# Kernel optimization log

Hardware: AMD Instinct MI355X
Metric: run time of the kernel (lower is better)

The kernel has to match this reference:

```python
import jax, jax.numpy as jnp
import numpy as np

ALPHA = 0.5
REG_RATIO = 0.5


def _xavier(key, shape):
    fan_in, fan_out = shape
    lim = np.sqrt(6.0 / (fan_in + fan_out))
    return jax.random.uniform(key, shape, minval=-lim, maxval=lim, dtype=jnp.float32)


def setup_inputs() -> dict:
    key = jax.random.key(0)
    ks = jax.random.split(key, 5)
    B, T, I, H, O = 128, 512, 4, 512, 3
    return {
        "x": jax.random.normal(ks[0], (B, T, I), dtype=jnp.float32),
        "h": jax.random.normal(ks[1], (B, H), dtype=jnp.float32),
        "W_rec": _xavier(ks[2], (H, H)),
        "W_in": _xavier(ks[3], (I, H)),
        "W_out": _xavier(ks[4], (H, O)),
        "bias_rec": jnp.zeros((H,), dtype=jnp.float32),
        "bias_in": jnp.zeros((H,), dtype=jnp.float32),
    }


def reference(x, h, W_rec, W_in, W_out, bias_rec, bias_in):
    # x: (B, T, I), h: (B, H)
    B, T, _ = x.shape
    H = h.shape[1]
    n_reg = round(H * REG_RATIO)
    alpha = jnp.asarray(ALPHA, x.dtype)
    # add_noise=False -> noise term is zero
    xt = jnp.swapaxes(x, 0, 1)                     # (T, B, I)
    flags = (jnp.arange(T) > 0).astype(x.dtype)    # z_old reg term skipped at t=0

    def step(carry, inp):
        h_prev, z_prev, reg = carry
        x_t, flag = inp
        # z = W_rec-recurrence + input drive (h_rec + h_in in the torch code)
        z_new = jnp.tanh(h_prev) @ W_rec + bias_rec + x_t @ W_in + bias_in  # (B, H)
        h_new = (1.0 - alpha) * h_prev + alpha * z_new
        # note: h_from_prev / (1 - alpha) == h_prev
        reg = (reg
               + jnp.sum((h_new[:, :n_reg] - h_prev[:, :n_reg]) ** 2)
               + flag * jnp.sum((z_new[:, :n_reg] - z_prev[:, :n_reg]) ** 2))
        out = h_new @ W_out                        # (B, O)
        return (h_new, z_new, reg), (h_new, out)

    init = (h, jnp.zeros_like(h), jnp.asarray(0.0, x.dtype))
    (_, _, reg), (hs, outs) = jax.lax.scan(step, init, (xt, flags))

    hidden_states = jnp.concatenate([h[None], hs], axis=0)  # (T+1, B, H)
    outputs = jnp.swapaxes(outs, 0, 1)                      # (B, T, O)
    tcr_reg = reg / T / B / n_reg
    return outputs, hidden_states, tcr_reg
```

## Files before the change

### kernel.cpp

```cpp
#include <hip/hip_runtime.h>
#include <math.h>


#define BB 128
#define TT 512
#define II 4
#define HH 512
#define OO 3
#define NREG_ 256

#define NTHREADS 512
#define MEMBERS 4
#define ROWS 2
#define NGROUPS 64
#define NBLOCKS (NGROUPS * MEMBERS)

typedef unsigned long long u64;
typedef unsigned int u32;

__device__ __forceinline__ u64 aload(const u64* p) {
    return __hip_atomic_load(p, __ATOMIC_RELAXED, __HIP_MEMORY_SCOPE_AGENT);
}
__device__ __forceinline__ void astore(u64* p, u64 v) {
    __hip_atomic_store(p, v, __ATOMIC_RELAXED, __HIP_MEMORY_SCOPE_AGENT);
}
__device__ __forceinline__ float rlane(float v, int l) {
    return __uint_as_float(__builtin_amdgcn_readlane(__float_as_uint(v), l));
}

#define R16(M) M(0) M(1) M(2) M(3) M(4) M(5) M(6) M(7) \
               M(8) M(9) M(10) M(11) M(12) M(13) M(14) M(15)

#define WLD(Q) \
    float4 wa##Q, wb##Q; \
    wa##Q.x = Wp[(size_t)(4*Q+0)*HH];      wa##Q.y = Wp[(size_t)(4*Q+1)*HH]; \
    wa##Q.z = Wp[(size_t)(4*Q+2)*HH];      wa##Q.w = Wp[(size_t)(4*Q+3)*HH]; \
    wb##Q.x = Wp[(size_t)(4*Q+0)*HH + 64]; wb##Q.y = Wp[(size_t)(4*Q+1)*HH + 64]; \
    wb##Q.z = Wp[(size_t)(4*Q+2)*HH + 64]; wb##Q.w = Wp[(size_t)(4*Q+3)*HH + 64];

#define MV(Q) \
    { float s0 = rlane(ar0, 4*Q+0), s1 = rlane(ar1, 4*Q+0); \
      acc00 = fmaf(s0, wa##Q.x, acc00); acc01 = fmaf(s0, wb##Q.x, acc01); \
      acc10 = fmaf(s1, wa##Q.x, acc10); acc11 = fmaf(s1, wb##Q.x, acc11); } \
    { float s0 = rlane(ar0, 4*Q+1), s1 = rlane(ar1, 4*Q+1); \
      acc00 = fmaf(s0, wa##Q.y, acc00); acc01 = fmaf(s0, wb##Q.y, acc01); \
      acc10 = fmaf(s1, wa##Q.y, acc10); acc11 = fmaf(s1, wb##Q.y, acc11); } \
    { float s0 = rlane(ar0, 4*Q+2), s1 = rlane(ar1, 4*Q+2); \
      acc00 = fmaf(s0, wa##Q.z, acc00); acc01 = fmaf(s0, wb##Q.z, acc01); \
      acc10 = fmaf(s1, wa##Q.z, acc10); acc11 = fmaf(s1, wb##Q.z, acc11); } \
    { float s0 = rlane(ar0, 4*Q+3), s1 = rlane(ar1, 4*Q+3); \
      acc00 = fmaf(s0, wa##Q.w, acc00); acc01 = fmaf(s0, wb##Q.w, acc01); \
      acc10 = fmaf(s1, wa##Q.w, acc10); acc11 = fmaf(s1, wb##Q.w, acc11); }

__global__ __launch_bounds__(NTHREADS, 2)
void rnn_main(const float* __restrict__ x,
              const float* __restrict__ h0,
              const float* __restrict__ W_rec,
              const float* __restrict__ W_in,
              const float* __restrict__ bias_rec,
              const float* __restrict__ bias_in,
              float* __restrict__ hidden,
              u64* __restrict__ abuf,
              float* __restrict__ partials)
{
    const int tid  = threadIdx.x;
    const int bid  = blockIdx.x;
    const int xcd  = bid & 7;
    const int onx  = bid >> 3;
    const int memb = onx & (MEMBERS - 1);
    const int group = xcd * 8 + (onx >> 2);
    const int r0   = group * ROWS;
    const int wid  = tid >> 6;
    const int lane = tid & 63;

    __shared__ float sc_s[ROWS][128][9];
    __shared__ float xbuf[ROWS * TT * II];
    __shared__ float win_s[II][128];
    __shared__ float ub_s[128];
    __shared__ float red_s[NTHREADS / 64];

    for (int idx = tid; idx < ROWS * TT * II; idx += NTHREADS) {
        int r = idx >> 11, rem = idx & (TT * II - 1);
        xbuf[idx] = x[(size_t)(r0 + r) * (TT * II) + rem];
    }
    if (tid < II * 128) {
        int i = tid >> 7, jj = tid & 127;
        win_s[i][jj] = W_in[i * HH + memb * 128 + jj];
    }
    if (tid < 128) {
        ub_s[tid] = bias_rec[memb * 128 + tid] + bias_in[memb * 128 + tid];
    }

    const float* Wp = W_rec + (size_t)(wid * 64) * HH + memb * 128 + lane;
    R16(WLD)

    const int fr  = tid >> 7;
    const int fj  = tid & 127;
    const int fjg = memb * 128 + fj;
    float hprev = 0.0f, zprev = 0.0f, racc = 0.0f;
    if (tid < ROWS * 128) {
        hprev = h0[(size_t)(r0 + fr) * HH + fjg];
        float a0v = tanhf(hprev);
        u64 pv = (u64)__float_as_uint(a0v) | ((u64)1u << 32);
        astore(&abuf[((size_t)(0 * BB + r0 + fr)) * HH + fjg], pv);
        hidden[(size_t)(r0 + fr) * HH + fjg] = hprev;
    }

#pragma unroll 1
    for (int t = 0; t < TT; ++t) {
        const int  slot = t & 1;
        const u32  tagc = (u32)(t + 1);
        const u32  tagp = (u32)(t + 2);

        const u64* p0 = abuf + ((size_t)(slot * BB + r0)) * HH + wid * 64 + lane;
        const u64* p1 = p0 + HH;
        u64 u0, u1;
        for (;;) {
            u0 = aload(p0);
            u1 = aload(p1);
            bool ok = ((u32)(u0 >> 32) == tagc) & ((u32)(u1 >> 32) == tagc);
            if (__all(ok)) break;
        }
        float ar0 = __uint_as_float((u32)u0);
        float ar1 = __uint_as_float((u32)u1);

        float acc00 = 0.0f, acc01 = 0.0f, acc10 = 0.0f, acc11 = 0.0f;
        R16(MV)

        sc_s[0][lane][wid]      = acc00;
        sc_s[0][lane + 64][wid] = acc01;
        sc_s[1][lane][wid]      = acc10;
        sc_s[1][lane + 64][wid] = acc11;
        __syncthreads();

        if (tid < ROWS * 128) {
            float q0 = sc_s[fr][fj][0], q1 = sc_s[fr][fj][1];
            float q2 = sc_s[fr][fj][2], q3 = sc_s[fr][fj][3];
            float q4 = sc_s[fr][fj][4], q5 = sc_s[fr][fj][5];
            float q6 = sc_s[fr][fj][6], q7 = sc_s[fr][fj][7];
            float z = ((q0 + q1) + (q2 + q3)) + ((q4 + q5) + (q6 + q7));
            z += ub_s[fj];
            const float* xr = &xbuf[fr * (TT * II) + t * II];
            z = fmaf(xr[0], win_s[0][fj], z);
            z = fmaf(xr[1], win_s[1][fj], z);
            z = fmaf(xr[2], win_s[2][fj], z);
            z = fmaf(xr[3], win_s[3][fj], z);
            float hn = 0.5f * hprev + 0.5f * z;
            float av = tanhf(hn);
            u64 pv = (u64)__float_as_uint(av) | ((u64)tagp << 32);
            astore(&abuf[((size_t)(((t + 1) & 1) * BB + r0 + fr)) * HH + fjg], pv);
            hidden[(size_t)(t + 1) * BB * HH + (size_t)(r0 + fr) * HH + fjg] = hn;
            if (fjg < NREG_) {
                float d1 = hn - hprev;
                racc = fmaf(d1, d1, racc);
                if (t > 0) { float d2 = z - zprev; racc = fmaf(d2, d2, racc); }
                zprev = z;
            }
            hprev = hn;
        }
        __syncthreads();
    }

    for (int off = 32; off; off >>= 1) racc += __shfl_down(racc, off);
    if ((tid & 63) == 0) red_s[tid >> 6] = racc;
    __syncthreads();
    if (tid == 0) {
        float s = 0.0f;
        for (int i = 0; i < NTHREADS / 64; ++i) s += red_s[i];
        partials[bid] = s;
    }
}

__global__ __launch_bounds__(256)
void rnn_out(const float* __restrict__ hidden,
             const float* __restrict__ W_out,
             float* __restrict__ outputs)
{
    __shared__ float wout_s[HH * OO];
    const int tid = threadIdx.x;
    for (int i = tid; i < HH * OO; i += 256) wout_s[i] = W_out[i];
    __syncthreads();

    const int gid  = blockIdx.x * 4 + (tid >> 6);
    const int lane = tid & 63;
    const int b = gid >> 9;
    const int t = gid & (TT - 1);
    const float* hp = hidden + (size_t)(t + 1) * BB * HH + (size_t)b * HH;

    float o0 = 0.0f, o1 = 0.0f, o2 = 0.0f;
#pragma unroll
    for (int q = 0; q < 8; ++q) {
        int k = lane + 64 * q;
        float hv = hp[k];
        o0 = fmaf(hv, wout_s[k * 3 + 0], o0);
        o1 = fmaf(hv, wout_s[k * 3 + 1], o1);
        o2 = fmaf(hv, wout_s[k * 3 + 2], o2);
    }
    for (int off = 32; off; off >>= 1) {
        o0 += __shfl_down(o0, off);
        o1 += __shfl_down(o1, off);
        o2 += __shfl_down(o2, off);
    }
    if (lane == 0) {
        float* op = outputs + (size_t)(b * TT + t) * OO;
        op[0] = o0; op[1] = o1; op[2] = o2;
    }
}

__global__ __launch_bounds__(256)
void rnn_tcr(const float* __restrict__ partials, float* __restrict__ tcr)
{
    __shared__ float red[4];
    const int tid = threadIdx.x;
    float v = partials[tid];
    for (int off = 32; off; off >>= 1) v += __shfl_down(v, off);
    if ((tid & 63) == 0) red[tid >> 6] = v;
    __syncthreads();
    if (tid == 0) {
        float s = red[0] + red[1] + red[2] + red[3];
        *tcr = s * (1.0f / ((float)TT * (float)BB * (float)NREG_));
    }
}

extern "C" void kernel_launch(void* const* d_in, const int* in_sizes, int n_in,
                              void* d_out, int out_size, void* d_ws, size_t ws_size,
                              hipStream_t stream)
{
    (void)in_sizes; (void)n_in; (void)out_size; (void)ws_size;

    const float* x     = (const float*)d_in[0];
    const float* h0    = (const float*)d_in[1];
    const float* W_rec = (const float*)d_in[2];
    const float* W_in  = (const float*)d_in[3];
    const float* W_out = (const float*)d_in[4];
    const float* brec  = (const float*)d_in[5];
    const float* bin   = (const float*)d_in[6];

    float* out     = (float*)d_out;
    float* outputs = out;
    float* hidden  = out + (size_t)BB * TT * OO;
    float* tcr     = out + (size_t)BB * TT * OO + (size_t)(TT + 1) * BB * HH;

    u64* abuf = (u64*)d_ws;
    const size_t abuf_bytes = (size_t)2 * BB * HH * sizeof(u64);
    float* partials = (float*)((char*)d_ws + abuf_bytes);

    (void)hipMemsetAsync(d_ws, 0, abuf_bytes, stream);

    void* args[] = { (void*)&x, (void*)&h0, (void*)&W_rec, (void*)&W_in,
                     (void*)&brec, (void*)&bin, (void*)&hidden,
                     (void*)&abuf, (void*)&partials };
    (void)hipLaunchCooperativeKernel((const void*)rnn_main,
                                     dim3(NBLOCKS), dim3(NTHREADS),
                                     args, 0, stream);

    rnn_out<<<dim3((BB * TT) / 4), dim3(256), 0, stream>>>(hidden, W_out, outputs);
    rnn_tcr<<<dim3(1), dim3(256), 0, stream>>>(partials, tcr);
}
```

Baseline: 1.212 ms.

## Use packed FMA for matvec, fast tanh, and double-buffer partials to drop a barrier

The inner mat-vec now uses inline v_pk_fma_f32 with a scalar pair of broadcast activations, halving the number of FMA instructions. tanhf is replaced by an exp/rcp approximation, which cuts latency on the serial critical path at some cost in accuracy. The shared-memory partial-sum buffer is double-buffered by timestep parity, so the second __syncthreads per step can be removed. The removal relies on the cross-block spin wait to keep warps from running more than one step ahead.

```diff
diff --git a/kernel.cpp b/kernel.cpp
--- a/kernel.cpp
+++ b/kernel.cpp
@@ -17,6 +17,7 @@
 
 typedef unsigned long long u64;
 typedef unsigned int u32;
+typedef __attribute__((ext_vector_type(2))) float f32x2;
 
 __device__ __forceinline__ u64 aload(const u64* p) {
     return __hip_atomic_load(p, __ATOMIC_RELAXED, __HIP_MEMORY_SCOPE_AGENT);
@@ -24,35 +25,35 @@
 __device__ __forceinline__ void astore(u64* p, u64 v) {
     __hip_atomic_store(p, v, __ATOMIC_RELAXED, __HIP_MEMORY_SCOPE_AGENT);
 }
-__device__ __forceinline__ float rlane(float v, int l) {
-    return __uint_as_float(__builtin_amdgcn_readlane(__float_as_uint(v), l));
+__device__ __forceinline__ float fast_tanh(float x) {
+    float ax = fabsf(x);
+    float e  = __expf(2.0f * ax);
+    float r  = 1.0f - 2.0f * __builtin_amdgcn_rcpf(e + 1.0f);
+    return copysignf(r, x);
 }
 
 #define R16(M) M(0) M(1) M(2) M(3) M(4) M(5) M(6) M(7) \
                M(8) M(9) M(10) M(11) M(12) M(13) M(14) M(15)
 
 #define WLD(Q) \
-    float4 wa##Q, wb##Q; \
-    wa##Q.x = Wp[(size_t)(4*Q+0)*HH];      wa##Q.y = Wp[(size_t)(4*Q+1)*HH]; \
-    wa##Q.z = Wp[(size_t)(4*Q+2)*HH];      wa##Q.w = Wp[(size_t)(4*Q+3)*HH]; \
-    wb##Q.x = Wp[(size_t)(4*Q+0)*HH + 64]; wb##Q.y = Wp[(size_t)(4*Q+1)*HH + 64]; \
-    wb##Q.z = Wp[(size_t)(4*Q+2)*HH + 64]; wb##Q.w = Wp[(size_t)(4*Q+3)*HH + 64];
-
-#define MV(Q) \
-    { float s0 = rlane(ar0, 4*Q+0), s1 = rlane(ar1, 4*Q+0); \
-      acc00 = fmaf(s0, wa##Q.x, acc00); acc01 = fmaf(s0, wb##Q.x, acc01); \
-      acc10 = fmaf(s1, wa##Q.x, acc10); acc11 = fmaf(s1, wb##Q.x, acc11); } \
-    { float s0 = rlane(ar0, 4*Q+1), s1 = rlane(ar1, 4*Q+1); \
-      acc00 = fmaf(s0, wa##Q.y, acc00); acc01 = fmaf(s0, wb##Q.y, acc01); \
-      acc10 = fmaf(s1, wa##Q.y, acc10); acc11 = fmaf(s1, wb##Q.y, acc11); } \
-    { float s0 = rlane(ar0, 4*Q+2), s1 = rlane(ar1, 4*Q+2); \
-      acc00 = fmaf(s0, wa##Q.z, acc00); acc01 = fmaf(s0, wb##Q.z, acc01); \
-      acc10 = fmaf(s1, wa##Q.z, acc10); acc11 = fmaf(s1, wb##Q.z, acc11); } \
-    { float s0 = rlane(ar0, 4*Q+3), s1 = rlane(ar1, 4*Q+3); \
-      acc00 = fmaf(s0, wa##Q.w, acc00); acc01 = fmaf(s0, wb##Q.w, acc01); \
-      acc10 = fmaf(s1, wa##Q.w, acc10); acc11 = fmaf(s1, wb##Q.w, acc11); }
-
-__global__ __launch_bounds__(NTHREADS, 2)
+    f32x2 w##Q##a, w##Q##b, w##Q##c, w##Q##d; \
+    w##Q##a.x = Wp[(size_t)(4*Q+0)*HH]; w##Q##a.y = Wp[(size_t)(4*Q+0)*HH+64]; \
+    w##Q##b.x = Wp[(size_t)(4*Q+1)*HH]; w##Q##b.y = Wp[(size_t)(4*Q+1)*HH+64]; \
+    w##Q##c.x = Wp[(size_t)(4*Q+2)*HH]; w##Q##c.y = Wp[(size_t)(4*Q+2)*HH+64]; \
+    w##Q##d.x = Wp[(size_t)(4*Q+3)*HH]; w##Q##d.y = Wp[(size_t)(4*Q+3)*HH+64];
+
+#define KSTEP(K, W) { \
+    u32 a0_ = __builtin_amdgcn_readlane(__float_as_uint(ar0), (K)); \
+    u32 a1_ = __builtin_amdgcn_readlane(__float_as_uint(ar1), (K)); \
+    u64 ab_ = (u64)a0_ | ((u64)a1_ << 32); \
+    asm("v_pk_fma_f32 %0, %2, %3, %0 op_sel_hi:[1,0,1]\n\t" \
+        "v_pk_fma_f32 %1, %2, %3, %1 op_sel:[0,1,0] op_sel_hi:[1,1,1]" \
+        : "+v"(accA), "+v"(accB) : "s"(ab_), "v"(W)); }
+
+#define MV(Q) KSTEP(4*Q+0, w##Q##a) KSTEP(4*Q+1, w##Q##b) \
+              KSTEP(4*Q+2, w##Q##c) KSTEP(4*Q+3, w##Q##d)
+
+__global__ __launch_bounds__(NTHREADS) __attribute__((amdgpu_waves_per_eu(2, 2)))
 void rnn_main(const float* __restrict__ x,
               const float* __restrict__ h0,
               const float* __restrict__ W_rec,
@@ -73,7 +74,7 @@
     const int wid  = tid >> 6;
     const int lane = tid & 63;
 
-    __shared__ float sc_s[ROWS][128][9];
+    __shared__ float sc_s[2][ROWS][128][9];
     __shared__ float xbuf[ROWS * TT * II];
     __shared__ float win_s[II][128];
     __shared__ float ub_s[128];
@@ -100,7 +101,7 @@
     float hprev = 0.0f, zprev = 0.0f, racc = 0.0f;
     if (tid < ROWS * 128) {
         hprev = h0[(size_t)(r0 + fr) * HH + fjg];
-        float a0v = tanhf(hprev);
+        float a0v = fast_tanh(hprev);
         u64 pv = (u64)__float_as_uint(a0v) | ((u64)1u << 32);
         astore(&abuf[((size_t)(0 * BB + r0 + fr)) * HH + fjg], pv);
         hidden[(size_t)(r0 + fr) * HH + fjg] = hprev;
@@ -108,9 +109,9 @@
 
 #pragma unroll 1
     for (int t = 0; t < TT; ++t) {
-        const int  slot = t & 1;
-        const u32  tagc = (u32)(t + 1);
-        const u32  tagp = (u32)(t + 2);
+        const int slot = t & 1;
+        const u32 tagc = (u32)(t + 1);
+        const u32 tagp = (u32)(t + 2);
 
         const u64* p0 = abuf + ((size_t)(slot * BB + r0)) * HH + wid * 64 + lane;
         const u64* p1 = p0 + HH;
@@ -124,20 +125,21 @@
         float ar0 = __uint_as_float((u32)u0);
         float ar1 = __uint_as_float((u32)u1);
 
-        float acc00 = 0.0f, acc01 = 0.0f, acc10 = 0.0f, acc11 = 0.0f;
+        f32x2 accA = {0.0f, 0.0f};
+        f32x2 accB = {0.0f, 0.0f};
         R16(MV)
 
-        sc_s[0][lane][wid]      = acc00;
-        sc_s[0][lane + 64][wid] = acc01;
-        sc_s[1][lane][wid]      = acc10;
-        sc_s[1][lane + 64][wid] = acc11;
+        sc_s[slot][0][lane][wid]      = accA.x;
+        sc_s[slot][1][lane][wid]      = accA.y;
+        sc_s[slot][0][lane + 64][wid] = accB.x;
+        sc_s[slot][1][lane + 64][wid] = accB.y;
         __syncthreads();
 
         if (tid < ROWS * 128) {
-            float q0 = sc_s[fr][fj][0], q1 = sc_s[fr][fj][1];
-            float q2 = sc_s[fr][fj][2], q3 = sc_s[fr][fj][3];
-            float q4 = sc_s[fr][fj][4], q5 = sc_s[fr][fj][5];
-            float q6 = sc_s[fr][fj][6], q7 = sc_s[fr][fj][7];
+            float q0 = sc_s[slot][fr][fj][0], q1 = sc_s[slot][fr][fj][1];
+            float q2 = sc_s[slot][fr][fj][2], q3 = sc_s[slot][fr][fj][3];
+            float q4 = sc_s[slot][fr][fj][4], q5 = sc_s[slot][fr][fj][5];
+            float q6 = sc_s[slot][fr][fj][6], q7 = sc_s[slot][fr][fj][7];
             float z = ((q0 + q1) + (q2 + q3)) + ((q4 + q5) + (q6 + q7));
             z += ub_s[fj];
             const float* xr = &xbuf[fr * (TT * II) + t * II];
@@ -146,7 +148,7 @@
             z = fmaf(xr[2], win_s[2][fj], z);
             z = fmaf(xr[3], win_s[3][fj], z);
             float hn = 0.5f * hprev + 0.5f * z;
-            float av = tanhf(hn);
+            float av = fast_tanh(hn);
             u64 pv = (u64)__float_as_uint(av) | ((u64)tagp << 32);
             astore(&abuf[((size_t)(((t + 1) & 1) * BB + r0 + fr)) * HH + fjg], pv);
             hidden[(size_t)(t + 1) * BB * HH + (size_t)(r0 + fr) * HH + fjg] = hn;
@@ -158,7 +160,6 @@
             }
             hprev = hn;
         }
-        __syncthreads();
     }
 
     for (int off = 32; off; off >>= 1) racc += __shfl_down(racc, off);
```

Measured after the change: 1.012 ms. 1.2x faster.
